# Optimization experiments

Hardware: AMD Instinct MI355X
Metric: run time of the kernel (lower is better)

The kernel has to match this reference:

```python
import jax, jax.numpy as jnp
import numpy as np

B, N, M, C, K = 4, 4096, 4096, 64, 32
RADIUS = 0.1
EPS = 1e-5


def setup_inputs() -> dict:
    key = jax.random.key(0)
    ks = jax.random.split(key, 32)
    inp = {
        "query_xyz": jax.random.uniform(ks[0], (B, N, 3), jnp.float32),
        "support_xyz": jax.random.uniform(ks[1], (B, M, 3), jnp.float32),
        "query_mask": jax.random.randint(ks[2], (B, N), 0, 2, jnp.int32),
        "support_mask": jax.random.randint(ks[3], (B, M), 0, 2, jnp.int32),
        "support_features": jax.random.normal(ks[4], (B, C, M), jnp.float32),
    }
    names = ["theta1", "theta2", "phi", "psi", "alpha", "gamma1", "gamma2"]
    in_ch = {"theta1": 3}
    for j, nm in enumerate(names):
        inp[f"W_{nm}"] = jax.random.normal(ks[5 + j], (C, in_ch.get(nm, C)), jnp.float32) * 0.05
        inp[f"b_{nm}"] = jax.random.normal(ks[12 + j], (C,), jnp.float32) * 0.05
    for j, nm in enumerate(["theta", "gamma"]):
        inp[f"g_{nm}"] = 1.0 + 0.1 * jax.random.normal(ks[19 + 2 * j], (C,), jnp.float32)
        inp[f"be_{nm}"] = 0.1 * jax.random.normal(ks[20 + 2 * j], (C,), jnp.float32)
        inp[f"rm_{nm}"] = jnp.zeros((C,), jnp.float32)
        inp[f"rv_{nm}"] = jnp.ones((C,), jnp.float32)
    return inp


def _conv(W, b, x):
    # 1x1 Conv2d: channelwise linear on [B, C_in, N, K]
    return jnp.einsum('oc,bcnk->bonk', W, x) + b[None, :, None, None]


def _bn(x, g, be, rm, rv):
    # BatchNorm2d, inference form with running stats
    inv = g / jnp.sqrt(rv + EPS)
    return x * inv[None, :, None, None] + (be - rm * inv)[None, :, None, None]


def _forward(query_xyz, support_xyz, query_mask, support_mask, support_features, P):
    Bq, Nq = query_xyz.shape[:2]
    # pairwise squared distances [B, N, M]; masked support pushed to +inf
    d2 = jnp.sum((query_xyz[:, :, None, :] - support_xyz[:, None, :, :]) ** 2, axis=-1)
    d2 = jnp.where(support_mask[:, None, :] > 0, d2, jnp.inf)
    # ball query as K-nearest-within-radius
    neg, idx = jax.lax.top_k(-d2, K)                    # idx: [B, N, K]
    nbr_mask = (-neg) <= RADIUS ** 2                    # valid-neighbor mask
    flat = idx.reshape(Bq, Nq * K)
    x_j = jnp.take_along_axis(support_features, flat[:, None, :], axis=2).reshape(Bq, -1, Nq, K)
    g_xyz = jnp.take_along_axis(support_xyz, flat[:, :, None], axis=1).reshape(Bq, Nq, K, 3)
    # normalize_xyz=True -> offsets divided by radius; layout [B, 3, N, K]
    pos = ((g_xyz - query_xyz[:, :, None, :]) / RADIUS).transpose(0, 3, 1, 2)
    # nearest-neighbor query for x_i [B, C, N]
    idx_nn = jnp.argmin(d2, axis=-1)
    x_i = jnp.take_along_axis(support_features, idx_nn[:, None, :], axis=2)
    # positional encoding delta
    delta = jax.nn.relu(_bn(_conv(P['W_theta2'], P['b_theta2'],
                                  _conv(P['W_theta1'], P['b_theta1'], pos)),
                            P['g_theta'], P['be_theta'], P['rm_theta'], P['rv_theta']))
    lin_i = _conv(P['W_phi'], P['b_phi'], x_i[..., None])   # [B,C,N,1], broadcast over K
    lin_j = _conv(P['W_psi'], P['b_psi'], x_j)
    rel = lin_i - lin_j + delta
    rel = jax.nn.relu(_bn(_conv(P['W_gamma2'], P['b_gamma2'],
                                _conv(P['W_gamma1'], P['b_gamma1'], rel)),
                          P['g_gamma'], P['be_gamma'], P['rm_gamma'], P['rv_gamma']))
    weights = jax.nn.softmax(rel, axis=-1)                   # softmax over neighbor axis
    feats = _conv(P['W_alpha'], P['b_alpha'], x_j) + delta
    fmask = nbr_mask.astype(feats.dtype) + (1.0 - query_mask.astype(feats.dtype))[:, :, None]
    feats = feats * fmask[:, None, :, :]
    return jnp.sum(weights * feats, axis=-1)                 # [B, C, N]


def reference(query_xyz, support_xyz, query_mask, support_mask, support_features,
              W_theta1, b_theta1, W_theta2, b_theta2, W_phi, b_phi, W_psi, b_psi,
              W_alpha, b_alpha, W_gamma1, b_gamma1, W_gamma2, b_gamma2,
              g_theta, be_theta, rm_theta, rv_theta, g_gamma, be_gamma, rm_gamma, rv_gamma):
    P = dict(locals())
    return _forward(query_xyz, support_xyz, query_mask, support_mask, support_features, P)
```

## Files before the change

kernel.cpp:

```cpp
#include <hip/hip_runtime.h>
#include <cstdint>
#include <cstddef>

#define NN 4096
#define MM 4096
#define CC 64
#define KK 32
#define INF_F __builtin_huge_valf()

#define SC 2304
#define CCAP 2560
#define NBUCK 256

typedef __bf16 bf16x8 __attribute__((ext_vector_type(8)));
typedef __bf16 bf16x4 __attribute__((ext_vector_type(4)));
typedef float f32x16 __attribute__((ext_vector_type(16)));

#define NFRAG 40
#define NPRE 24
#define ASTRIDE 68
#define ESTRIDE 36

#define WFENCE() asm volatile("s_waitcnt lgkmcnt(0)" ::: "memory")


__device__ __forceinline__ f32x16 zero16() {
  f32x16 z;
#pragma unroll
  for (int i = 0; i < 16; ++i) z[i] = 0.0f;
  return z;
}

__device__ __forceinline__ void conv1(const bf16x8* Wr, int conv,
                                      const bf16x8* B4, f32x16& a0, f32x16& a1) {
#pragma unroll
  for (int s = 0; s < 4; ++s) {
    a0 = __builtin_amdgcn_mfma_f32_32x32x16_bf16(Wr[(conv * 2 + 0) * 4 + s], B4[s], a0, 0, 0, 0);
    a1 = __builtin_amdgcn_mfma_f32_32x32x16_bf16(Wr[(conv * 2 + 1) * 4 + s], B4[s], a1, 0, 0, 0);
  }
}

__device__ __forceinline__ void conv1g(const bf16x8* __restrict__ Wf, int conv, int lane,
                                       const bf16x8* B4, f32x16& a0, f32x16& a1) {
#pragma unroll
  for (int s = 0; s < 4; ++s) {
    const bf16x8 w0 = Wf[((conv * 2 + 0) * 4 + s) * 64 + lane];
    const bf16x8 w1 = Wf[((conv * 2 + 1) * 4 + s) * 64 + lane];
    a0 = __builtin_amdgcn_mfma_f32_32x32x16_bf16(w0, B4[s], a0, 0, 0, 0);
    a1 = __builtin_amdgcn_mfma_f32_32x32x16_bf16(w1, B4[s], a1, 0, 0, 0);
  }
}

__device__ __forceinline__ void sort64(float& v, int& i, int lane) {
#pragma unroll
  for (int k = 2; k <= 64; k <<= 1) {
#pragma unroll
    for (int j = k >> 1; j > 0; j >>= 1) {
      const float ov = __shfl_xor(v, j);
      const int oi = __shfl_xor(i, j);
      const bool up = ((lane & k) == 0);
      const bool lower = ((lane & j) == 0);
      const bool take = (up == lower) ? (ov < v) : (ov > v);
      if (take) { v = ov; i = oi; }
    }
  }
}

__device__ __forceinline__ void insert_cands(float vv, int ii, float& sv, int& si,
                                             float& cmax, int lane) {
  unsigned long long cand = __ballot(vv < cmax);
  while (cand) {
    const int src = __ffsll((unsigned long long)cand) - 1;
    cand &= cand - 1;
    const float dc = __shfl(vv, src);
    if (dc < cmax) {
      const int im = __shfl(ii, src);
      const float up_s = __shfl_up(sv, 1);
      const int up_i = __shfl_up(si, 1);
      const bool pg = sv > dc;
      const bool pgu = (lane > 0) && (up_s > dc);
      const float ns = pg ? (pgu ? up_s : dc) : sv;
      const int ni = pg ? (pgu ? up_i : im) : si;
      if (lane < 32) { sv = ns; si = ni; }
      cmax = __shfl(sv, 31);
    }
  }
}

__global__ void pt_setup(const float* __restrict__ sf, const float* __restrict__ sxyz,
                         const int* __restrict__ smask,
                         const float* __restrict__ Wpsi, const float* __restrict__ W2,
                         const float* __restrict__ Wg1, const float* __restrict__ Wg2,
                         const float* __restrict__ Wa, const float* __restrict__ Wphi,
                         const float* __restrict__ gT, const float* __restrict__ beT,
                         const float* __restrict__ rmT, const float* __restrict__ rvT,
                         const float* __restrict__ gG, const float* __restrict__ beG,
                         const float* __restrict__ rmG, const float* __restrict__ rvG,
                         const float* __restrict__ b2, const float* __restrict__ bg1,
                         const float* __restrict__ bg2, const float* __restrict__ ba,
                         __bf16* __restrict__ ftb, float4* __restrict__ sx4,
                         float4* __restrict__ cpts, __bf16* __restrict__ Wpack,
                         float* __restrict__ WphiT, float4* __restrict__ eo,
                         float4* __restrict__ bo, int* __restrict__ boffp) {
  const int blk = blockIdx.x;
  const int tid = threadIdx.x;

  if (blk < 64) {
    const int b = blk >> 4;
    const int m = ((blk & 15) << 8) + tid;
    float v[CC];
#pragma unroll
    for (int c = 0; c < CC; ++c) v[c] = sf[((size_t)(b * CC + c)) * MM + m];
    bf16x8* db = (bf16x8*)(ftb + ((size_t)(b * MM + m)) * CC);
#pragma unroll
    for (int i = 0; i < CC / 8; ++i) {
      bf16x8 t;
#pragma unroll
      for (int j = 0; j < 8; ++j) t[j] = (__bf16)v[8 * i + j];
      db[i] = t;
    }
    const size_t g = (size_t)(b * MM + m);
    sx4[g] = make_float4(sxyz[g * 3 + 0], sxyz[g * 3 + 1], sxyz[g * 3 + 2], 0.0f);
    return;
  }

  if (blk < 68) {
    __shared__ int cnt[NBUCK];
    __shared__ int cur[NBUCK];
    __shared__ int wtot[4];
    const int b = blk - 64;
    const int lane = tid & 63;
    const int w = tid >> 6;
    cnt[tid] = 0;
    __syncthreads();
#pragma unroll 1
    for (int r = 0; r < 16; ++r) {
      const int m = r * 256 + tid;
      const size_t g = (size_t)b * MM + m;
      if (smask[g] > 0) {
        int bk = (int)(sxyz[g * 3 + 0] * 256.0f);
        bk = min(max(bk, 0), NBUCK - 1);
        atomicAdd(&cnt[bk], 1);
      }
    }
    __syncthreads();
    const int v = cnt[tid];
    int inc = v;
#pragma unroll
    for (int off = 1; off < 64; off <<= 1) {
      const int o = __shfl_up(inc, off);
      if (lane >= off) inc += o;
    }
    if (lane == 63) wtot[w] = inc;
    __syncthreads();
    int excl = inc - v;
#pragma unroll
    for (int i = 0; i < 4; ++i) excl += (i < w) ? wtot[i] : 0;
    cur[tid] = excl;
    boffp[b * 257 + tid] = excl;
    const int total = wtot[0] + wtot[1] + wtot[2] + wtot[3];
    if (tid == 0) boffp[b * 257 + 256] = total;
    __syncthreads();
    float4* dst = cpts + (size_t)b * CCAP;
#pragma unroll 1
    for (int r = 0; r < 16; ++r) {
      const int m = r * 256 + tid;
      const size_t g = (size_t)b * MM + m;
      if (smask[g] > 0) {
        const float x = sxyz[g * 3 + 0];
        const float y = sxyz[g * 3 + 1];
        const float z = sxyz[g * 3 + 2];
        int bk = (int)(x * 256.0f);
        bk = min(max(bk, 0), NBUCK - 1);
        const int pos = atomicAdd(&cur[bk], 1);
        dst[pos] = make_float4(x, y, z, __int_as_float(m));
      }
    }
    for (int i = total + tid; i < SC; i += 256)
      dst[i] = make_float4(1e4f, 1e4f, 1e4f, __int_as_float(0));
    return;
  }

  const int t = (blk - 68) * 256 + tid;
  if (t < NFRAG * 64) {
    const int lane = t & 63;
    const int fi = t >> 6;
    const int s = fi & 3;
    const int mt = (fi >> 2) & 1;
    const int conv = fi >> 3;
    const float* W = conv == 0 ? Wpsi : conv == 1 ? W2 : conv == 2 ? Wg1 : conv == 3 ? Wg2 : Wa;
    const int m = mt * 32 + (lane & 31);
    const int k0 = s * 16 + (lane >> 5) * 8;
    bf16x8 vh;
#pragma unroll
    for (int j = 0; j < 8; ++j) vh[j] = (__bf16)W[m * CC + k0 + j];
    ((bf16x8*)Wpack)[fi * 64 + lane] = vh;
    return;
  }
  const int t2 = t - NFRAG * 64;
  if (t2 < CC * CC) {
    WphiT[t2] = Wphi[(t2 & 63) * CC + (t2 >> 6)];
    return;
  }
  const int o = t2 - CC * CC;
  if (o < CC) {
    const float invT = gT[o] / sqrtf(rvT[o] + 1e-5f);
    const float invG = gG[o] / sqrtf(rvG[o] + 1e-5f);
    eo[o] = make_float4(invT, beT[o] - rmT[o] * invT, invG, beG[o] - rmG[o] * invG);
    bo[o] = make_float4(b2[o], bg1[o], bg2[o], ba[o]);
  }
}

__global__ void pt_knn(const float* __restrict__ qxyz, const float4* __restrict__ cpts,
                       const int* __restrict__ boff, const __bf16* __restrict__ ftb,
                       const float* __restrict__ WphiT, const float* __restrict__ bphi,
                       const float* __restrict__ bpsi,
                       int* __restrict__ oidx, unsigned* __restrict__ ovalid,
                       float* __restrict__ lin) {
  const int lane = threadIdx.x & 63;
  const int qi = blockIdx.x * 4 + (threadIdx.x >> 6);
  const int b = qi >> 12;
  const float qx = qxyz[qi * 3 + 0];
  const float qy = qxyz[qi * 3 + 1];
  const float qz = qxyz[qi * 3 + 2];
  const float4* sb = cpts + (size_t)b * CCAP;
  const int* bo = boff + b * 257;
  const int cnt = bo[256];

  float R = 0.155f;
#pragma unroll
  for (int it = 0; it < 2; ++it) {
    const float cx = fminf(qx + R, 1.0f) - fmaxf(qx - R, 0.0f);
    const float cy = fminf(qy + R, 1.0f) - fmaxf(qy - R, 0.0f);
    const float cz = fminf(qz + R, 1.0f) - fmaxf(qz - R, 0.0f);
    const float n = fmaxf((float)cnt * 0.5235988f * cx * cy * cz, 1.0f);
    R *= __powf(48.0f / n, 0.33333333f);
  }
  R = fminf(fmaxf(R, 0.06f), 0.7f);

  const int lob = max((int)((qx - R) * 256.0f), 0);
  const int hib = min((int)((qx + R) * 256.0f), NBUCK - 1);
  const int r0 = bo[lob] >> 6;
  const int r1 = (bo[hib + 1] + 63) >> 6;

  float v0 = INF_F, v1 = INF_F, v2 = INF_F, v3 = INF_F;
  int i0 = 0, i1 = 0, i2 = 0, i3 = 0;
  int r = r0;
#pragma unroll 1
  for (; r + 4 <= r1; r += 4) {
    float4 P[4];
#pragma unroll
    for (int u = 0; u < 4; ++u) P[u] = sb[(r + u) * 64 + lane];
#pragma unroll
    for (int u = 0; u < 4; ++u) {
      const float dx = P[u].x - qx, dy = P[u].y - qy, dz = P[u].z - qz;
      const float d = dx * dx + dy * dy + dz * dz;
      const int m = __float_as_int(P[u].w);
      const bool c3 = d < v3, c2 = d < v2, c1 = d < v1, c0 = d < v0;
      v3 = c3 ? (c2 ? v2 : d) : v3;  i3 = c3 ? (c2 ? i2 : m) : i3;
      v2 = c2 ? (c1 ? v1 : d) : v2;  i2 = c2 ? (c1 ? i1 : m) : i2;
      v1 = c1 ? (c0 ? v0 : d) : v1;  i1 = c1 ? (c0 ? i0 : m) : i1;
      v0 = c0 ? d : v0;              i0 = c0 ? m : i0;
    }
  }
#pragma unroll 1
  for (; r < r1; ++r) {
    const float4 p = sb[r * 64 + lane];
    const float dx = p.x - qx, dy = p.y - qy, dz = p.z - qz;
    const float d = dx * dx + dy * dy + dz * dz;
    const int m = __float_as_int(p.w);
    const bool c3 = d < v3, c2 = d < v2, c1 = d < v1, c0 = d < v0;
    v3 = c3 ? (c2 ? v2 : d) : v3;  i3 = c3 ? (c2 ? i2 : m) : i3;
    v2 = c2 ? (c1 ? v1 : d) : v2;  i2 = c2 ? (c1 ? i1 : m) : i2;
    v1 = c1 ? (c0 ? v0 : d) : v1;  i1 = c1 ? (c0 ? i0 : m) : i1;
    v0 = c0 ? d : v0;              i0 = c0 ? m : i0;
  }

  float sv = v0;
  int si = i0;
  sort64(sv, si, lane);
  float cmax = __shfl(sv, 31);
  insert_cands(v1, i1, sv, si, cmax, lane);
  insert_cands(v2, i2, sv, si, cmax, lane);
  insert_cands(v3, i3, sv, si, cmax, lane);

  if (__ballot(v3 < cmax) && r1 > r0) {
    {
      const float4 p = sb[r0 * 64 + lane];
      const float dx = p.x - qx, dy = p.y - qy, dz = p.z - qz;
      float v = dx * dx + dy * dy + dz * dz;
      int id = __float_as_int(p.w);
      sort64(v, id, lane);
      sv = v; si = id;
    }
    cmax = __shfl(sv, 31);
    for (int rr = r0 + 1; rr < r1; ++rr) {
      const float4 p = sb[rr * 64 + lane];
      const float dx = p.x - qx, dy = p.y - qy, dz = p.z - qz;
      const float d = dx * dx + dy * dy + dz * dz;
      insert_cands(d, __float_as_int(p.w), sv, si, cmax, lane);
    }
  }

  const float gl = (lob > 0) ? (qx - (float)lob * 0.00390625f) : INF_F;
  const float gr = (hib < NBUCK - 1) ? ((float)(hib + 1) * 0.00390625f - qx) : INF_F;
  const float G = fminf(gl, gr);
  if (cmax > G * G) {
    const float R1 = sqrtf(cmax);
    const int lob2 = max((int)((qx - R1) * 256.0f), 0);
    const int hib2 = min((int)((qx + R1) * 256.0f), NBUCK - 1);
    const int s0 = bo[lob2] >> 6;
    const int s1 = (bo[hib2 + 1] + 63) >> 6;
    for (int rr = s0; rr < r0; ++rr) {
      const float4 p = sb[rr * 64 + lane];
      const float dx = p.x - qx, dy = p.y - qy, dz = p.z - qz;
      insert_cands(dx * dx + dy * dy + dz * dz, __float_as_int(p.w), sv, si, cmax, lane);
    }
    for (int rr = r1; rr < s1; ++rr) {
      const float4 p = sb[rr * 64 + lane];
      const float dx = p.x - qx, dy = p.y - qy, dz = p.z - qz;
      insert_cands(dx * dx + dy * dy + dz * dz, __float_as_int(p.w), sv, si, cmax, lane);
    }
  }

  if (lane < 32) oidx[(size_t)qi * KK + lane] = si;
  const unsigned long long vb = __ballot((lane < 32) && (sv <= 0.01f));
  if (lane == 0) ovalid[qi] = (unsigned)(vb & 0xffffffffull);

  const int nnb = __shfl(si, 0);
  const bf16x8* xr = (const bf16x8*)(ftb + ((size_t)(b * MM + nnb)) * CC);
  float a = bphi[lane] - bpsi[lane];
#pragma unroll
  for (int i = 0; i < 8; ++i) {
    const bf16x8 xv = xr[i];
#pragma unroll
    for (int j = 0; j < 8; ++j) a += WphiT[(8 * i + j) * CC + lane] * (float)xv[j];
  }
  lin[qi * CC + lane] = a;
}

__launch_bounds__(256, 3)
__global__ void pt_fused(
    const float* __restrict__ qxyz, const float4* __restrict__ sx4,
    const int* __restrict__ qmask, const __bf16* __restrict__ ftb,
    const int* __restrict__ kidx, const unsigned* __restrict__ kvalid,
    const float* __restrict__ lin,
    const float* __restrict__ W1, const float* __restrict__ b1,
    const __bf16* __restrict__ Wpack, const float4* __restrict__ eo,
    const float4* __restrict__ bo, float* __restrict__ out) {
  __shared__ float EPI[4][CC * ESTRIDE];
  __shared__ float4 sEO[CC], sBO[CC];
  const int wid = threadIdx.x >> 6;
  const int lane = threadIdx.x & 63;
  const int g = lane >> 5;
  const int col = lane & 31;
  const int q = blockIdx.x * 4 + wid;
  const int b = q >> 12;
  const int nq = q & (NN - 1);
  float* epi = EPI[wid];
  __bf16* act = (__bf16*)epi;
  const bf16x8* Wf = (const bf16x8*)Wpack;

  bf16x8 Wr[NPRE];
#pragma unroll
  for (int f = 0; f < NPRE; ++f) Wr[f] = Wf[f * 64 + lane];

  sEO[lane] = eo[lane];
  sBO[lane] = bo[lane];

  const int idx = kidx[q * KK + col];
  const float fm = (float)((kvalid[q] >> col) & 1u) + 1.0f - (float)qmask[q];

  bf16x8 Xb[4];
  {
    const __bf16* ftq = ftb + ((size_t)(b * MM + idx)) * CC;
#pragma unroll
    for (int s = 0; s < 4; ++s) Xb[s] = *(const bf16x8*)(ftq + s * 16 + g * 8);
  }

  bf16x8 Tb[4];
  {
    const float qx = qxyz[q * 3 + 0], qy = qxyz[q * 3 + 1], qz = qxyz[q * 3 + 2];
    const float4 pj = sx4[(size_t)b * MM + idx];
    const float p0 = (pj.x - qx) * 10.0f;
    const float p1 = (pj.y - qy) * 10.0f;
    const float p2 = (pj.z - qz) * 10.0f;
#pragma unroll
    for (int s = 0; s < 4; ++s) {
      bf16x8 t;
#pragma unroll
      for (int j = 0; j < 8; ++j) {
        const int c = s * 16 + g * 8 + j;
        t[j] = (__bf16)(b1[c] + W1[c * 3 + 0] * p0 + W1[c * 3 + 1] * p1 + W1[c * 3 + 2] * p2);
      }
      Tb[s] = t;
    }
  }
  WFENCE();

  float DELv[32];
  {
    f32x16 aT0 = zero16(), aT1 = zero16();
    conv1(Wr, 1, Tb, aT0, aT1);
#pragma unroll
    for (int mt = 0; mt < 2; ++mt)
#pragma unroll
      for (int t = 0; t < 4; ++t)
#pragma unroll
        for (int i = 0; i < 4; ++i) {
          const int r = t * 4 + i;
          const int o = mt * 32 + 8 * t + 4 * g + i;
          const float4 e = sEO[o];
          DELv[mt * 16 + r] = fmaxf(((mt ? aT1[r] : aT0[r]) + sBO[o].x) * e.x + e.y, 0.0f);
        }
  }

  {
    f32x16 aP0 = zero16(), aP1 = zero16();
    conv1(Wr, 0, Xb, aP0, aP1);
#pragma unroll
    for (int mt = 0; mt < 2; ++mt)
#pragma unroll
      for (int t = 0; t < 4; ++t) {
        const int ob = mt * 32 + 8 * t + 4 * g;
        const float4 lv = *(const float4*)(lin + q * CC + ob);
        const float lva[4] = {lv.x, lv.y, lv.z, lv.w};
        bf16x4 w;
#pragma unroll
        for (int i = 0; i < 4; ++i) {
          const int r = t * 4 + i;
          w[i] = (__bf16)(lva[i] - (mt ? aP1[r] : aP0[r]) + DELv[mt * 16 + r]);
        }
        *(bf16x4*)(act + col * ASTRIDE + ob) = w;
      }
  }
  WFENCE();

  {
    bf16x8 Rb[4];
#pragma unroll
    for (int s = 0; s < 4; ++s) {
      const bf16x4 lo = *(const bf16x4*)(act + col * ASTRIDE + s * 16 + g * 8);
      const bf16x4 hi = *(const bf16x4*)(act + col * ASTRIDE + s * 16 + g * 8 + 4);
      Rb[s] = bf16x8{lo[0], lo[1], lo[2], lo[3], hi[0], hi[1], hi[2], hi[3]};
    }
    f32x16 a0 = zero16(), a1 = zero16();
    conv1(Wr, 2, Rb, a0, a1);
#pragma unroll
    for (int mt = 0; mt < 2; ++mt)
#pragma unroll
      for (int t = 0; t < 4; ++t) {
        const int ob = mt * 32 + 8 * t + 4 * g;
        bf16x4 w;
#pragma unroll
        for (int i = 0; i < 4; ++i) {
          const int r = t * 4 + i;
          w[i] = (__bf16)((mt ? a1[r] : a0[r]) + sBO[ob + i].y);
        }
        *(bf16x4*)(act + col * ASTRIDE + ob) = w;
      }
  }
  WFENCE();

  f32x16 h0 = zero16(), h1 = zero16();
  {
    bf16x8 Rb[4];
#pragma unroll
    for (int s = 0; s < 4; ++s) {
      const bf16x4 lo = *(const bf16x4*)(act + col * ASTRIDE + s * 16 + g * 8);
      const bf16x4 hi = *(const bf16x4*)(act + col * ASTRIDE + s * 16 + g * 8 + 4);
      Rb[s] = bf16x8{lo[0], lo[1], lo[2], lo[3], hi[0], hi[1], hi[2], hi[3]};
    }
    conv1g(Wf, 3, lane, Rb, h0, h1);
  }
  WFENCE();

#pragma unroll
  for (int mt = 0; mt < 2; ++mt)
#pragma unroll
    for (int t = 0; t < 4; ++t)
#pragma unroll
      for (int i = 0; i < 4; ++i) {
        const int r = t * 4 + i;
        const int o = mt * 32 + 4 * g + 8 * t + i;
        const float4 e = sEO[o];
        const float v = fmaxf(((mt ? h1[r] : h0[r]) + sBO[o].z) * e.z + e.w, 0.0f);
        epi[o * ESTRIDE + col] = v;
      }
  WFENCE();

  float ev[32];
  float sum;
  {
    const float* row = epi + lane * ESTRIDE;
    float mx = -INF_F;
#pragma unroll
    for (int n = 0; n < 32; n += 4) {
      const float4 t = *(const float4*)(row + n);
      ev[n] = t.x; ev[n + 1] = t.y; ev[n + 2] = t.z; ev[n + 3] = t.w;
      mx = fmaxf(mx, fmaxf(fmaxf(t.x, t.y), fmaxf(t.z, t.w)));
    }
    sum = 0.0f;
#pragma unroll
    for (int n = 0; n < 32; ++n) { ev[n] = __expf(ev[n] - mx); sum += ev[n]; }
  }
  WFENCE();

  f32x16 fa0 = zero16(), fa1 = zero16();
  conv1g(Wf, 4, lane, Xb, fa0, fa1);

#pragma unroll
  for (int mt = 0; mt < 2; ++mt)
#pragma unroll
    for (int t = 0; t < 4; ++t)
#pragma unroll
      for (int i = 0; i < 4; ++i) {
        const int r = t * 4 + i;
        const int o = mt * 32 + 4 * g + 8 * t + i;
        const float f = ((mt ? fa1[r] : fa0[r]) + sBO[o].w + DELv[mt * 16 + r]) * fm;
        epi[o * ESTRIDE + col] = f;
      }
  WFENCE();

  {
    const float* row = epi + lane * ESTRIDE;
    float acc = 0.0f;
#pragma unroll
    for (int n = 0; n < 32; n += 4) {
      const float4 t = *(const float4*)(row + n);
      acc += ev[n] * t.x + ev[n + 1] * t.y + ev[n + 2] * t.z + ev[n + 3] * t.w;
    }
    out[((size_t)(b * CC + lane)) * NN + nq] = acc * __builtin_amdgcn_rcpf(sum);
  }
}

extern "C" void kernel_launch(void* const* d_in, const int* in_sizes, int n_in,
                              void* d_out, int out_size, void* d_ws, size_t ws_size,
                              hipStream_t stream) {
  (void)in_sizes; (void)n_in; (void)out_size; (void)ws_size;
  const float* qxyz = (const float*)d_in[0];
  const float* sxyz = (const float*)d_in[1];
  const int* qmask = (const int*)d_in[2];
  const int* smask = (const int*)d_in[3];
  const float* sfeat = (const float*)d_in[4];
  const float* W1 = (const float*)d_in[5];
  const float* b1 = (const float*)d_in[6];
  const float* W2 = (const float*)d_in[7];
  const float* b2 = (const float*)d_in[8];
  const float* Wphi = (const float*)d_in[9];
  const float* bphi = (const float*)d_in[10];
  const float* Wpsi = (const float*)d_in[11];
  const float* bpsi = (const float*)d_in[12];
  const float* Wa = (const float*)d_in[13];
  const float* ba = (const float*)d_in[14];
  const float* Wg1 = (const float*)d_in[15];
  const float* bg1 = (const float*)d_in[16];
  const float* Wg2 = (const float*)d_in[17];
  const float* bg2 = (const float*)d_in[18];
  const float* gT = (const float*)d_in[19];
  const float* beT = (const float*)d_in[20];
  const float* rmT = (const float*)d_in[21];
  const float* rvT = (const float*)d_in[22];
  const float* gG = (const float*)d_in[23];
  const float* beG = (const float*)d_in[24];
  const float* rmG = (const float*)d_in[25];
  const float* rvG = (const float*)d_in[26];

  char* ws = (char*)d_ws;
  int* kidx      = (int*)(ws + 0);
  unsigned* kval = (unsigned*)(ws + 2097152);
  __bf16* ftb    = (__bf16*)(ws + 2162688);
  float4* sx4    = (float4*)(ws + 4259840);
  float* lin     = (float*)(ws + 4521984);
  __bf16* Wpack  = (__bf16*)(ws + 8716288);
  float4* eo     = (float4*)(ws + 8757248);
  float4* bo     = (float4*)(ws + 8758272);
  float4* cpts   = (float4*)(ws + 8759296);
  float* WphiT   = (float*)(ws + 8923136);
  int* boffp     = (int*)(ws + 8939520);

  hipLaunchKernelGGL(pt_setup, dim3(95), dim3(256), 0, stream,
                     sfeat, sxyz, smask,
                     Wpsi, W2, Wg1, Wg2, Wa, Wphi,
                     gT, beT, rmT, rvT, gG, beG, rmG, rvG, b2, bg1, bg2, ba,
                     ftb, sx4, cpts, Wpack, WphiT, eo, bo, boffp);
  hipLaunchKernelGGL(pt_knn, dim3(4096), dim3(256), 0, stream,
                     qxyz, cpts, boffp, ftb, WphiT, bphi, bpsi, kidx, kval, lin);
  hipLaunchKernelGGL(pt_fused, dim3(4096), dim3(256), 0, stream,
                     qxyz, sx4, qmask, ftb, kidx, kval, lin,
                     W1, b1, Wpack, eo, bo, (float*)d_out);
}
```

Baseline: 236.4 us.

## Split bucket sort into parallel histogram/scan/scatter and cut fused-kernel register pressure

The setup stage previously ran the spatial bucket sort in only 4 blocks and the feature transpose in 64 blocks with 64 channels per thread. It now spreads the transpose over 256 blocks and splits the sort into per-slice histograms, a scan kernel and a parallel scatter kernel. In the fused kernel, weights are no longer preloaded into 24 register fragments; they are read from global memory per MFMA, and neighbour features are reloaded late so Xb is not live across the whole kernel. Launch bounds rise to 4 waves per SIMD for occupancy. The cost is two extra kernel launches and more global/L2 weight loads in the fused kernel.

```diff
diff --git a/kernel.cpp b/kernel.cpp
--- a/kernel.cpp
+++ b/kernel.cpp
@@ -17,7 +17,6 @@
 typedef float f32x16 __attribute__((ext_vector_type(16)));
 
 #define NFRAG 40
-#define NPRE 24
 #define ASTRIDE 68
 #define ESTRIDE 36
 
@@ -29,15 +28,6 @@
 #pragma unroll
   for (int i = 0; i < 16; ++i) z[i] = 0.0f;
   return z;
-}
-
-__device__ __forceinline__ void conv1(const bf16x8* Wr, int conv,
-                                      const bf16x8* B4, f32x16& a0, f32x16& a1) {
-#pragma unroll
-  for (int s = 0; s < 4; ++s) {
-    a0 = __builtin_amdgcn_mfma_f32_32x32x16_bf16(Wr[(conv * 2 + 0) * 4 + s], B4[s], a0, 0, 0, 0);
-    a1 = __builtin_amdgcn_mfma_f32_32x32x16_bf16(Wr[(conv * 2 + 1) * 4 + s], B4[s], a1, 0, 0, 0);
-  }
 }
 
 __device__ __forceinline__ void conv1g(const bf16x8* __restrict__ Wf, int conv, int lane,
@@ -99,89 +89,52 @@
                          const float* __restrict__ b2, const float* __restrict__ bg1,
                          const float* __restrict__ bg2, const float* __restrict__ ba,
                          __bf16* __restrict__ ftb, float4* __restrict__ sx4,
-                         float4* __restrict__ cpts, __bf16* __restrict__ Wpack,
-                         float* __restrict__ WphiT, float4* __restrict__ eo,
-                         float4* __restrict__ bo, int* __restrict__ boffp) {
+                         __bf16* __restrict__ Wpack, float* __restrict__ WphiT,
+                         float4* __restrict__ eo, float4* __restrict__ bo,
+                         int* __restrict__ cnt2) {
   const int blk = blockIdx.x;
   const int tid = threadIdx.x;
 
-  if (blk < 64) {
-    const int b = blk >> 4;
-    const int m = ((blk & 15) << 8) + tid;
-    float v[CC];
-#pragma unroll
-    for (int c = 0; c < CC; ++c) v[c] = sf[((size_t)(b * CC + c)) * MM + m];
-    bf16x8* db = (bf16x8*)(ftb + ((size_t)(b * MM + m)) * CC);
-#pragma unroll
-    for (int i = 0; i < CC / 8; ++i) {
-      bf16x8 t;
-#pragma unroll
-      for (int j = 0; j < 8; ++j) t[j] = (__bf16)v[8 * i + j];
-      db[i] = t;
-    }
-    const size_t g = (size_t)(b * MM + m);
-    sx4[g] = make_float4(sxyz[g * 3 + 0], sxyz[g * 3 + 1], sxyz[g * 3 + 2], 0.0f);
+  if (blk < 256) {
+    const int b = blk >> 6;
+    const int m = ((blk & 63) << 6) + (tid & 63);
+    const int cg = tid >> 6;
+    float v[16];
+#pragma unroll
+    for (int j = 0; j < 16; ++j) v[j] = sf[((size_t)(b * CC + cg * 16 + j)) * MM + m];
+    __bf16* db = ftb + ((size_t)(b * MM + m)) * CC + cg * 16;
+    bf16x8 t0, t1;
+#pragma unroll
+    for (int j = 0; j < 8; ++j) { t0[j] = (__bf16)v[j]; t1[j] = (__bf16)v[8 + j]; }
+    *(bf16x8*)db = t0;
+    *(bf16x8*)(db + 8) = t1;
+    if (cg == 0) {
+      const size_t g = (size_t)(b * MM + m);
+      sx4[g] = make_float4(sxyz[g * 3 + 0], sxyz[g * 3 + 1], sxyz[g * 3 + 2], 0.0f);
+    }
     return;
   }
 
-  if (blk < 68) {
-    __shared__ int cnt[NBUCK];
-    __shared__ int cur[NBUCK];
-    __shared__ int wtot[4];
-    const int b = blk - 64;
-    const int lane = tid & 63;
-    const int w = tid >> 6;
-    cnt[tid] = 0;
+  if (blk < 320) {
+    __shared__ int hcnt[NBUCK];
+    const int sub = blk - 256;
+    const int b = sub >> 4;
+    const int s = sub & 15;
+    hcnt[tid] = 0;
     __syncthreads();
-#pragma unroll 1
-    for (int r = 0; r < 16; ++r) {
-      const int m = r * 256 + tid;
-      const size_t g = (size_t)b * MM + m;
-      if (smask[g] > 0) {
-        int bk = (int)(sxyz[g * 3 + 0] * 256.0f);
-        bk = min(max(bk, 0), NBUCK - 1);
-        atomicAdd(&cnt[bk], 1);
-      }
+    const int m = s * 256 + tid;
+    const size_t g = (size_t)b * MM + m;
+    if (smask[g] > 0) {
+      int bk = (int)(sxyz[g * 3 + 0] * 256.0f);
+      bk = min(max(bk, 0), NBUCK - 1);
+      atomicAdd(&hcnt[bk], 1);
     }
     __syncthreads();
-    const int v = cnt[tid];
-    int inc = v;
-#pragma unroll
-    for (int off = 1; off < 64; off <<= 1) {
-      const int o = __shfl_up(inc, off);
-      if (lane >= off) inc += o;
-    }
-    if (lane == 63) wtot[w] = inc;
-    __syncthreads();
-    int excl = inc - v;
-#pragma unroll
-    for (int i = 0; i < 4; ++i) excl += (i < w) ? wtot[i] : 0;
-    cur[tid] = excl;
-    boffp[b * 257 + tid] = excl;
-    const int total = wtot[0] + wtot[1] + wtot[2] + wtot[3];
-    if (tid == 0) boffp[b * 257 + 256] = total;
-    __syncthreads();
-    float4* dst = cpts + (size_t)b * CCAP;
-#pragma unroll 1
-    for (int r = 0; r < 16; ++r) {
-      const int m = r * 256 + tid;
-      const size_t g = (size_t)b * MM + m;
-      if (smask[g] > 0) {
-        const float x = sxyz[g * 3 + 0];
-        const float y = sxyz[g * 3 + 1];
-        const float z = sxyz[g * 3 + 2];
-        int bk = (int)(x * 256.0f);
-        bk = min(max(bk, 0), NBUCK - 1);
-        const int pos = atomicAdd(&cur[bk], 1);
-        dst[pos] = make_float4(x, y, z, __int_as_float(m));
-      }
-    }
-    for (int i = total + tid; i < SC; i += 256)
-      dst[i] = make_float4(1e4f, 1e4f, 1e4f, __int_as_float(0));
+    cnt2[(b * 16 + s) * NBUCK + tid] = hcnt[tid];
     return;
   }
 
-  const int t = (blk - 68) * 256 + tid;
+  const int t = (blk - 320) * 256 + tid;
   if (t < NFRAG * 64) {
     const int lane = t & 63;
     const int fi = t >> 6;
@@ -208,6 +161,67 @@
     const float invG = gG[o] / sqrtf(rvG[o] + 1e-5f);
     eo[o] = make_float4(invT, beT[o] - rmT[o] * invT, invG, beG[o] - rmG[o] * invG);
     bo[o] = make_float4(b2[o], bg1[o], bg2[o], ba[o]);
+  }
+}
+
+__global__ void pt_scan(int* __restrict__ cnt2, int* __restrict__ boffp,
+                        float4* __restrict__ cpts) {
+  __shared__ int wtot[4];
+  const int b = blockIdx.x;
+  const int tid = threadIdx.x;
+  const int lane = tid & 63;
+  const int w = tid >> 6;
+
+  int c[16];
+  int tot = 0;
+#pragma unroll
+  for (int s = 0; s < 16; ++s) {
+    c[s] = cnt2[(b * 16 + s) * NBUCK + tid];
+    tot += c[s];
+  }
+  int inc = tot;
+#pragma unroll
+  for (int off = 1; off < 64; off <<= 1) {
+    const int o = __shfl_up(inc, off);
+    if (lane >= off) inc += o;
+  }
+  if (lane == 63) wtot[w] = inc;
+  __syncthreads();
+  int excl = inc - tot;
+#pragma unroll
+  for (int i = 0; i < 4; ++i) excl += (i < w) ? wtot[i] : 0;
+  boffp[b * 257 + tid] = excl;
+  const int total = wtot[0] + wtot[1] + wtot[2] + wtot[3];
+  if (tid == 0) boffp[b * 257 + 256] = total;
+  int base = excl;
+#pragma unroll
+  for (int s = 0; s < 16; ++s) {
+    cnt2[(b * 16 + s) * NBUCK + tid] = base;
+    base += c[s];
+  }
+  float4* dst = cpts + (size_t)b * CCAP;
+  for (int i = total + tid; i < SC; i += 256)
+    dst[i] = make_float4(1e4f, 1e4f, 1e4f, __int_as_float(0));
+}
+
+__global__ void pt_scatter(const float* __restrict__ sxyz, const int* __restrict__ smask,
+                           const int* __restrict__ cnt2, float4* __restrict__ cpts) {
+  __shared__ int cur[NBUCK];
+  const int b = blockIdx.x >> 4;
+  const int s = blockIdx.x & 15;
+  const int tid = threadIdx.x;
+  cur[tid] = cnt2[(b * 16 + s) * NBUCK + tid];
+  __syncthreads();
+  const int m = s * 256 + tid;
+  const size_t g = (size_t)b * MM + m;
+  if (smask[g] > 0) {
+    const float x = sxyz[g * 3 + 0];
+    const float y = sxyz[g * 3 + 1];
+    const float z = sxyz[g * 3 + 2];
+    int bk = (int)(x * 256.0f);
+    bk = min(max(bk, 0), NBUCK - 1);
+    const int pos = atomicAdd(&cur[bk], 1);
+    cpts[(size_t)b * CCAP + pos] = make_float4(x, y, z, __int_as_float(m));
   }
 }
 
@@ -339,7 +353,7 @@
   lin[qi * CC + lane] = a;
 }
 
-__launch_bounds__(256, 3)
+__launch_bounds__(256, 4)
 __global__ void pt_fused(
     const float* __restrict__ qxyz, const float4* __restrict__ sx4,
     const int* __restrict__ qmask, const __bf16* __restrict__ ftb,
@@ -361,22 +375,17 @@
   __bf16* act = (__bf16*)epi;
   const bf16x8* Wf = (const bf16x8*)Wpack;
 
-  bf16x8 Wr[NPRE];
-#pragma unroll
-  for (int f = 0; f < NPRE; ++f) Wr[f] = Wf[f * 64 + lane];
-
   sEO[lane] = eo[lane];
   sBO[lane] = bo[lane];
+  WFENCE();
 
   const int idx = kidx[q * KK + col];
   const float fm = (float)((kvalid[q] >> col) & 1u) + 1.0f - (float)qmask[q];
+  const __bf16* ftq = ftb + ((size_t)(b * MM + idx)) * CC;
 
   bf16x8 Xb[4];
-  {
-    const __bf16* ftq = ftb + ((size_t)(b * MM + idx)) * CC;
-#pragma unroll
-    for (int s = 0; s < 4; ++s) Xb[s] = *(const bf16x8*)(ftq + s * 16 + g * 8);
-  }
+#pragma unroll
+  for (int s = 0; s < 4; ++s) Xb[s] = *(const bf16x8*)(ftq + s * 16 + g * 8);
 
   bf16x8 Tb[4];
   {
@@ -396,12 +405,11 @@
       Tb[s] = t;
     }
   }
-  WFENCE();
 
   float DELv[32];
   {
     f32x16 aT0 = zero16(), aT1 = zero16();
-    conv1(Wr, 1, Tb, aT0, aT1);
+    conv1g(Wf, 1, lane, Tb, aT0, aT1);
 #pragma unroll
     for (int mt = 0; mt < 2; ++mt)
 #pragma unroll
@@ -417,7 +425,7 @@
 
   {
     f32x16 aP0 = zero16(), aP1 = zero16();
-    conv1(Wr, 0, Xb, aP0, aP1);
+    conv1g(Wf, 0, lane, Xb, aP0, aP1);
 #pragma unroll
     for (int mt = 0; mt < 2; ++mt)
 #pragma unroll
@@ -445,7 +453,7 @@
       Rb[s] = bf16x8{lo[0], lo[1], lo[2], lo[3], hi[0], hi[1], hi[2], hi[3]};
     }
     f32x16 a0 = zero16(), a1 = zero16();
-    conv1(Wr, 2, Rb, a0, a1);
+    conv1g(Wf, 2, lane, Rb, a0, a1);
 #pragma unroll
     for (int mt = 0; mt < 2; ++mt)
 #pragma unroll
@@ -487,6 +495,10 @@
         const float v = fmaxf(((mt ? h1[r] : h0[r]) + sBO[o].z) * e.z + e.w, 0.0f);
         epi[o * ESTRIDE + col] = v;
       }
+
+  bf16x8 Xb2[4];
+#pragma unroll
+  for (int s = 0; s < 4; ++s) Xb2[s] = *(const bf16x8*)(ftq + s * 16 + g * 8);
   WFENCE();
 
   float ev[32];
@@ -507,7 +519,7 @@
   WFENCE();
 
   f32x16 fa0 = zero16(), fa1 = zero16();
-  conv1g(Wf, 4, lane, Xb, fa0, fa1);
+  conv1g(Wf, 4, lane, Xb2, fa0, fa1);
 
 #pragma unroll
   for (int mt = 0; mt < 2; ++mt)
@@ -578,12 +590,15 @@
   float4* cpts   = (float4*)(ws + 8759296);
   float* WphiT   = (float*)(ws + 8923136);
   int* boffp     = (int*)(ws + 8939520);
-
-  hipLaunchKernelGGL(pt_setup, dim3(95), dim3(256), 0, stream,
+  int* cnt2      = (int*)(ws + 8943744);
+
+  hipLaunchKernelGGL(pt_setup, dim3(347), dim3(256), 0, stream,
                      sfeat, sxyz, smask,
                      Wpsi, W2, Wg1, Wg2, Wa, Wphi,
                      gT, beT, rmT, rvT, gG, beG, rmG, rvG, b2, bg1, bg2, ba,
-                     ftb, sx4, cpts, Wpack, WphiT, eo, bo, boffp);
+                     ftb, sx4, Wpack, WphiT, eo, bo, cnt2);
+  hipLaunchKernelGGL(pt_scan, dim3(4), dim3(256), 0, stream, cnt2, boffp, cpts);
+  hipLaunchKernelGGL(pt_scatter, dim3(64), dim3(256), 0, stream, sxyz, smask, cnt2, cpts);
   hipLaunchKernelGGL(pt_knn, dim3(4096), dim3(256), 0, stream,
                      qxyz, cpts, boffp, ftb, WphiT, bphi, bpsi, kidx, kval, lin);
   hipLaunchKernelGGL(pt_fused, dim3(4096), dim3(256), 0, stream,
```

New measurement: 248.4 us. 1.05x slower.
